# Kernel optimization log

Hardware: AMD Instinct MI355X
Metric: run time of the kernel (lower is better)

## Reference

```python
import jax, jax.numpy as jnp
import numpy as np

NQ = 6       # total qubits
NF = 4
NL = 2       # layers
B = 65536    # batch
WEIGHT_INIT_STD = 0.01


def _apply_1q(state, gate, w):
    """Apply a 2x2 gate (shared (2,2) or per-sample (B,2,2)) to qubit w.
    state: (B, 2,2,2,2,2,2) complex64, axis w+1 is qubit w (PennyLane wire order)."""
    ax = w + 1
    s = jnp.moveaxis(state, ax, -1)
    shp = s.shape
    s = s.reshape(shp[0], -1, 2)
    if gate.ndim == 2:
        s = jnp.einsum('ij,bkj->bki', gate, s)
    else:
        s = jnp.einsum('bij,bkj->bki', gate, s)
    return jnp.moveaxis(s.reshape(shp), -1, ax)


def _cnot(state, c, t):
    """CNOT with control c, target t: flip target axis where control bit = 1."""
    ac, at = c + 1, t + 1
    s0 = jax.lax.index_in_dim(state, 0, ac, keepdims=True)
    s1 = jnp.flip(jax.lax.index_in_dim(state, 1, ac, keepdims=True), axis=at)
    return jnp.concatenate([s0, s1], axis=ac)


def _ry(theta):
    ct = jnp.cos(theta * 0.5)
    st = jnp.sin(theta * 0.5)
    return jnp.stack([jnp.stack([ct, -st]), jnp.stack([st, ct])]).astype(jnp.complex64)


def _circuit(x, weights, ancilla_bias):
    b = x.shape[0]
    state = jnp.zeros((b,) + (2,) * NQ, jnp.complex64)
    state = state.at[(slice(None),) + (0,) * NQ].set(1.0)  # |000000>
    # RX(x[:, w]) encoding on qubits 0..3 (batched gates)
    half = x.astype(jnp.float32) * 0.5
    c = jnp.cos(half).astype(jnp.complex64)
    s = (-1j) * jnp.sin(half).astype(jnp.complex64)
    for w in range(NF):
        g = jnp.stack([jnp.stack([c[:, w], s[:, w]], -1),
                       jnp.stack([s[:, w], c[:, w]], -1)], -2)  # (B,2,2)
        state = _apply_1q(state, g, w)
    # RY ancilla init on qubits 4, 5
    state = _apply_1q(state, _ry(ancilla_bias[0]), 4)
    state = _apply_1q(state, _ry(ancilla_bias[1]), 5)
    # entangling layers: CNOT ring then RY rotations
    for l in range(weights.shape[0]):
        for w in range(NQ):
            state = _cnot(state, w, (w + 1) % NQ)
        for w in range(NQ):
            state = _apply_1q(state, _ry(weights[l, w]), w)
    # <Z_w> for w in 0..3
    p = state.real ** 2 + state.imag ** 2  # (B,2,...,2)
    outs = []
    for w in range(NF):
        pw = p.sum(axis=tuple(a for a in range(1, NQ + 1) if a != w + 1))  # (B,2)
        outs.append(pw[:, 0] - pw[:, 1])
    return jnp.stack(outs, -1).astype(jnp.float32)  # (B, 4)


def setup_inputs() -> dict:
    key = jax.random.key(0)
    k1, k2 = jax.random.split(key)
    x = jax.random.normal(k1, (B, NF), jnp.float32)
    weights = jax.random.normal(k2, (NL, NQ), jnp.float32) * WEIGHT_INIT_STD
    ancilla_bias = jnp.zeros((2,), jnp.float32)
    return {"x": x, "weights": weights, "ancilla_bias": ancilla_bias}


def reference(x, weights, ancilla_bias):
    return _circuit(x, weights, ancilla_bias)
```

## Files before the change

### kernel.cpp

```cpp
#include <hip/hip_runtime.h>


#define NQ 6
#define NF 4
#define NL 2
#define NS 64

__global__ __launch_bounds__(256) void qcirc6_kernel(
    const float* __restrict__ x,
    const float* __restrict__ weights,
    const float* __restrict__ bias,
    float* __restrict__ out,
    int B)
{
    int i = blockIdx.x * blockDim.x + threadIdx.x;
    if (i >= B) return;

    float4 xv = reinterpret_cast<const float4*>(x)[i];
    float xs[NF] = {xv.x, xv.y, xv.z, xv.w};

    float re[NS], im[NS];
    #pragma unroll
    for (int k = 0; k < NS; ++k) { re[k] = 0.0f; im[k] = 0.0f; }
    re[0] = 1.0f;

    #pragma unroll
    for (int w = 0; w < NF; ++w) {
        float s, c;
        __sincosf(xs[w] * 0.5f, &s, &c);
        const int m = 1 << (5 - w);
        #pragma unroll
        for (int k = 0; k < NS; ++k) {
            if (k & m) continue;
            const int j = k | m;
            const float a0r = re[k], a0i = im[k];
            const float a1r = re[j], a1i = im[j];
            re[k] =  c * a0r + s * a1i;
            im[k] =  c * a0i - s * a1r;
            re[j] =  s * a0i + c * a1r;
            im[j] = -s * a0r + c * a1i;
        }
    }

    #pragma unroll
    for (int q = 0; q < 2; ++q) {
        float st, ct;
        __sincosf(bias[q] * 0.5f, &st, &ct);
        const int m = 1 << (5 - (4 + q));
        #pragma unroll
        for (int k = 0; k < NS; ++k) {
            if (k & m) continue;
            const int j = k | m;
            const float a0r = re[k], a0i = im[k];
            const float a1r = re[j], a1i = im[j];
            re[k] = ct * a0r - st * a1r;
            im[k] = ct * a0i - st * a1i;
            re[j] = st * a0r + ct * a1r;
            im[j] = st * a0i + ct * a1i;
        }
    }

    #pragma unroll
    for (int l = 0; l < NL; ++l) {
        #pragma unroll
        for (int w = 0; w < NQ; ++w) {
            const int cm = 1 << (5 - w);
            const int tm = 1 << (5 - ((w + 1) % NQ));
            #pragma unroll
            for (int k = 0; k < NS; ++k) {
                if ((k & cm) && !(k & tm)) {
                    const int j = k | tm;
                    float t;
                    t = re[k]; re[k] = re[j]; re[j] = t;
                    t = im[k]; im[k] = im[j]; im[j] = t;
                }
            }
        }
        #pragma unroll
        for (int w = 0; w < NQ; ++w) {
            float st, ct;
            __sincosf(weights[l * NQ + w] * 0.5f, &st, &ct);
            const int m = 1 << (5 - w);
            #pragma unroll
            for (int k = 0; k < NS; ++k) {
                if (k & m) continue;
                const int j = k | m;
                const float a0r = re[k], a0i = im[k];
                const float a1r = re[j], a1i = im[j];
                re[k] = ct * a0r - st * a1r;
                im[k] = ct * a0i - st * a1i;
                re[j] = st * a0r + ct * a1r;
                im[j] = st * a0i + ct * a1i;
            }
        }
    }

    float z0 = 0.f, z1 = 0.f, z2 = 0.f, z3 = 0.f;
    #pragma unroll
    for (int k = 0; k < NS; ++k) {
        const float p = re[k] * re[k] + im[k] * im[k];
        z0 += (k & 32) ? -p : p;
        z1 += (k & 16) ? -p : p;
        z2 += (k &  8) ? -p : p;
        z3 += (k &  4) ? -p : p;
    }
    reinterpret_cast<float4*>(out)[i] = make_float4(z0, z1, z2, z3);
}

extern "C" void kernel_launch(void* const* d_in, const int* in_sizes, int n_in,
                              void* d_out, int out_size, void* d_ws, size_t ws_size,
                              hipStream_t stream) {
    const float* x       = (const float*)d_in[0];
    const float* weights = (const float*)d_in[1];
    const float* bias    = (const float*)d_in[2];
    float* out = (float*)d_out;
    const int B = in_sizes[0] / NF;
    qcirc6_kernel<<<(B + 255) / 256, 256, 0, stream>>>(x, weights, bias, out, B);
}
```

Baseline: 63.89 us.

## Split each 64-amplitude state across four lanes using cross-lane shuffles

Each sample's 6-qubit state vector is now spread over four threads. Every thread holds 16 amplitudes, with qubits 4 and 5 mapped to the lane index. Gates on the lane qubits and the CNOTs that cross lanes become shuffles, and the Z expectations are reduced across the four lanes before each lane writes one output. The aim is to cut per-thread register pressure, raising occupancy and parallelism, at the cost of many extra shuffle instructions and four times as many threads.

```diff
diff --git a/kernel.cpp b/kernel.cpp
--- a/kernel.cpp
+++ b/kernel.cpp
@@ -1,110 +1,144 @@
 #include <hip/hip_runtime.h>
 
 
-#define NQ 6
-#define NF 4
 #define NL 2
-#define NS 64
 
-__global__ __launch_bounds__(256) void qcirc6_kernel(
+__global__ __launch_bounds__(256) void qcirc6_l4_kernel(
     const float* __restrict__ x,
     const float* __restrict__ weights,
     const float* __restrict__ bias,
     float* __restrict__ out,
     int B)
 {
-    int i = blockIdx.x * blockDim.x + threadIdx.x;
-    if (i >= B) return;
+    const int gid = blockIdx.x * blockDim.x + threadIdx.x;
+    const int sample = gid >> 2;
+    if (sample >= B) return;
+    const int lane = threadIdx.x & 63;
+    const int sub = lane & 3;
 
-    float4 xv = reinterpret_cast<const float4*>(x)[i];
-    float xs[NF] = {xv.x, xv.y, xv.z, xv.w};
+    const float4 xv = reinterpret_cast<const float4*>(x)[sample];
+    const float xs[4] = {xv.x, xv.y, xv.z, xv.w};
 
-    float re[NS], im[NS];
+    float re[16], im[16];
     #pragma unroll
-    for (int k = 0; k < NS; ++k) { re[k] = 0.0f; im[k] = 0.0f; }
-    re[0] = 1.0f;
+    for (int t = 0; t < 16; ++t) { re[t] = 0.0f; im[t] = 0.0f; }
+    re[0] = (sub == 0) ? 1.0f : 0.0f;
 
     #pragma unroll
-    for (int w = 0; w < NF; ++w) {
+    for (int w = 0; w < 4; ++w) {
         float s, c;
         __sincosf(xs[w] * 0.5f, &s, &c);
-        const int m = 1 << (5 - w);
+        const int m = 1 << (3 - w);
         #pragma unroll
-        for (int k = 0; k < NS; ++k) {
-            if (k & m) continue;
-            const int j = k | m;
-            const float a0r = re[k], a0i = im[k];
+        for (int t = 0; t < 16; ++t) {
+            if (t & m) continue;
+            const int j = t | m;
+            const float a0r = re[t], a0i = im[t];
             const float a1r = re[j], a1i = im[j];
-            re[k] =  c * a0r + s * a1i;
-            im[k] =  c * a0i - s * a1r;
+            re[t] =  c * a0r + s * a1i;
+            im[t] =  c * a0i - s * a1r;
             re[j] =  s * a0i + c * a1r;
             im[j] = -s * a0r + c * a1i;
         }
     }
 
-    #pragma unroll
-    for (int q = 0; q < 2; ++q) {
-        float st, ct;
-        __sincosf(bias[q] * 0.5f, &st, &ct);
-        const int m = 1 << (5 - (4 + q));
+    auto ry_lane = [&](float st, float ct, int lmask) {
+        const float sg = (sub & lmask) ? st : -st;
         #pragma unroll
-        for (int k = 0; k < NS; ++k) {
-            if (k & m) continue;
-            const int j = k | m;
-            const float a0r = re[k], a0i = im[k];
+        for (int t = 0; t < 16; ++t) {
+            const float pr = __shfl_xor(re[t], lmask, 64);
+            const float pi = __shfl_xor(im[t], lmask, 64);
+            re[t] = ct * re[t] + sg * pr;
+            im[t] = ct * im[t] + sg * pi;
+        }
+    };
+
+    auto ry_local = [&](float st, float ct, int m) {
+        #pragma unroll
+        for (int t = 0; t < 16; ++t) {
+            if (t & m) continue;
+            const int j = t | m;
+            const float a0r = re[t], a0i = im[t];
             const float a1r = re[j], a1i = im[j];
-            re[k] = ct * a0r - st * a1r;
-            im[k] = ct * a0i - st * a1i;
+            re[t] = ct * a0r - st * a1r;
+            im[t] = ct * a0i - st * a1i;
             re[j] = st * a0r + ct * a1r;
             im[j] = st * a0i + ct * a1i;
         }
+    };
+
+    auto cnot_local = [&](int cm, int tm) {
+        #pragma unroll
+        for (int t = 0; t < 16; ++t) {
+            if ((t & cm) && !(t & tm)) {
+                const int j = t | tm;
+                float tmp;
+                tmp = re[t]; re[t] = re[j]; re[j] = tmp;
+                tmp = im[t]; im[t] = im[j]; im[j] = tmp;
+            }
+        }
+    };
+
+    {
+        float st, ct;
+        __sincosf(bias[0] * 0.5f, &st, &ct);
+        ry_lane(st, ct, 2);
+        __sincosf(bias[1] * 0.5f, &st, &ct);
+        ry_lane(st, ct, 1);
     }
+
+    const int perm45 = (sub & 2) ? (lane ^ 1) : lane;
+    const bool c50 = (sub & 1) != 0;
 
     #pragma unroll
     for (int l = 0; l < NL; ++l) {
+        cnot_local(8, 4);
+        cnot_local(4, 2);
+        cnot_local(2, 1);
         #pragma unroll
-        for (int w = 0; w < NQ; ++w) {
-            const int cm = 1 << (5 - w);
-            const int tm = 1 << (5 - ((w + 1) % NQ));
-            #pragma unroll
-            for (int k = 0; k < NS; ++k) {
-                if ((k & cm) && !(k & tm)) {
-                    const int j = k | tm;
-                    float t;
-                    t = re[k]; re[k] = re[j]; re[j] = t;
-                    t = im[k]; im[k] = im[j]; im[j] = t;
-                }
-            }
+        for (int t = 1; t < 16; t += 2) {
+            re[t] = __shfl_xor(re[t], 2, 64);
+            im[t] = __shfl_xor(im[t], 2, 64);
         }
         #pragma unroll
-        for (int w = 0; w < NQ; ++w) {
-            float st, ct;
-            __sincosf(weights[l * NQ + w] * 0.5f, &st, &ct);
-            const int m = 1 << (5 - w);
-            #pragma unroll
-            for (int k = 0; k < NS; ++k) {
-                if (k & m) continue;
-                const int j = k | m;
-                const float a0r = re[k], a0i = im[k];
-                const float a1r = re[j], a1i = im[j];
-                re[k] = ct * a0r - st * a1r;
-                im[k] = ct * a0i - st * a1i;
-                re[j] = st * a0r + ct * a1r;
-                im[j] = st * a0i + ct * a1i;
-            }
+        for (int t = 0; t < 16; ++t) {
+            re[t] = __shfl(re[t], perm45, 64);
+            im[t] = __shfl(im[t], perm45, 64);
         }
+        #pragma unroll
+        for (int t = 0; t < 8; ++t) {
+            const int j = t | 8;
+            float a, b;
+            a = re[t]; b = re[j];
+            re[t] = c50 ? b : a;  re[j] = c50 ? a : b;
+            a = im[t]; b = im[j];
+            im[t] = c50 ? b : a;  im[j] = c50 ? a : b;
+        }
+        float st, ct;
+        __sincosf(weights[l * 6 + 0] * 0.5f, &st, &ct); ry_local(st, ct, 8);
+        __sincosf(weights[l * 6 + 1] * 0.5f, &st, &ct); ry_local(st, ct, 4);
+        __sincosf(weights[l * 6 + 2] * 0.5f, &st, &ct); ry_local(st, ct, 2);
+        __sincosf(weights[l * 6 + 3] * 0.5f, &st, &ct); ry_local(st, ct, 1);
+        __sincosf(weights[l * 6 + 4] * 0.5f, &st, &ct); ry_lane(st, ct, 2);
+        __sincosf(weights[l * 6 + 5] * 0.5f, &st, &ct); ry_lane(st, ct, 1);
     }
 
     float z0 = 0.f, z1 = 0.f, z2 = 0.f, z3 = 0.f;
     #pragma unroll
-    for (int k = 0; k < NS; ++k) {
-        const float p = re[k] * re[k] + im[k] * im[k];
-        z0 += (k & 32) ? -p : p;
-        z1 += (k & 16) ? -p : p;
-        z2 += (k &  8) ? -p : p;
-        z3 += (k &  4) ? -p : p;
+    for (int t = 0; t < 16; ++t) {
+        const float p = re[t] * re[t] + im[t] * im[t];
+        z0 += (t & 8) ? -p : p;
+        z1 += (t & 4) ? -p : p;
+        z2 += (t & 2) ? -p : p;
+        z3 += (t & 1) ? -p : p;
     }
-    reinterpret_cast<float4*>(out)[i] = make_float4(z0, z1, z2, z3);
+    z0 += __shfl_xor(z0, 1, 64); z0 += __shfl_xor(z0, 2, 64);
+    z1 += __shfl_xor(z1, 1, 64); z1 += __shfl_xor(z1, 2, 64);
+    z2 += __shfl_xor(z2, 1, 64); z2 += __shfl_xor(z2, 2, 64);
+    z3 += __shfl_xor(z3, 1, 64); z3 += __shfl_xor(z3, 2, 64);
+
+    const float zsel = (sub == 0) ? z0 : (sub == 1) ? z1 : (sub == 2) ? z2 : z3;
+    out[sample * 4 + sub] = zsel;
 }
 
 extern "C" void kernel_launch(void* const* d_in, const int* in_sizes, int n_in,
@@ -114,6 +148,7 @@
     const float* weights = (const float*)d_in[1];
     const float* bias    = (const float*)d_in[2];
     float* out = (float*)d_out;
-    const int B = in_sizes[0] / NF;
-    qcirc6_kernel<<<(B + 255) / 256, 256, 0, stream>>>(x, weights, bias, out, B);
+    const int B = in_sizes[0] / 4;
+    const int threads = B * 4;
+    qcirc6_l4_kernel<<<(threads + 255) / 256, 256, 0, stream>>>(x, weights, bias, out, B);
 }
```

After: 72.43 us. 1.13x slower.
